# Performance work log

Hardware: AMD Instinct MI355X
Metric: run time of the kernel (lower is better)

## Reference

```python
import jax, jax.numpy as jnp
import numpy as np

EPS = 1e-5
HEADS = 4


def _ln(x, s, b):
    m = jnp.mean(x, axis=-1, keepdims=True)
    v = jnp.mean(jnp.square(x - m), axis=-1, keepdims=True)
    return (x - m) * jax.lax.rsqrt(v + EPS) * s + b


def _gru(x, Wg, bg, Wcx, bcx, Wch, bch):
    # In this GRUCell the gates depend only on the inputs, so the gate and
    # candidate_x matmuls are precomputed over all timesteps; only the
    # (reset*h) @ Wch matmul is sequential.
    gx = jax.nn.sigmoid(x @ Wg + bg)   # [B,S,2H]
    cx = x @ Wcx + bcx                 # [B,S,H]
    H = Wch.shape[0]

    def step(h, gc):
        g, c = gc
        r, u = jnp.split(g, 2, axis=-1)
        cand = jnp.tanh(c + (r * h) @ Wch + bch)
        h_new = u * h + (1.0 - u) * cand
        return h_new, h_new

    h0 = jnp.zeros((x.shape[0], H), x.dtype)
    _, ys = jax.lax.scan(step, h0, (gx.transpose(1, 0, 2), cx.transpose(1, 0, 2)))
    return ys.transpose(1, 0, 2)


def _attn(x, s, b, Wq, bq, Wk, bk, Wv, bv, Wo, bo):
    skip = x
    xn = _ln(x, s, b)
    B, S, _ = xn.shape
    QKV = Wq.shape[1]
    hd = QKV // HEADS
    q = (xn @ Wq + bq).reshape(B, S, HEADS, hd)
    k = (xn @ Wk + bk).reshape(B, S, HEADS, hd)
    v = (xn @ Wv + bv).reshape(B, S, HEADS, hd)
    scores = jnp.einsum('bqhd,bkhd->bhqk', q, k) / jnp.sqrt(jnp.asarray(hd, x.dtype))
    probs = jax.nn.softmax(scores, axis=-1)
    o = jnp.einsum('bhqk,bkhd->bqhd', probs, v).reshape(B, S, QKV)
    return o @ Wo + bo + skip


def _forward(x_cgm, x_other, W_in, b_in, ln0_s, ln0_b,
             g0_Wg, g0_bg, g0_Wcx, g0_bcx, g0_Wch, g0_bch, ln1_s, ln1_b,
             g1_Wg, g1_bg, g1_Wcx, g1_bcx, g1_Wch, g1_bch, ln2_s, ln2_b,
             aln_s, aln_b, Wq, bq, Wk, bk, Wv, bv, Wo, bo,
             Wd1, bd1, lnd1_s, lnd1_b, Wd2, bd2, lnd2_s, lnd2_b, Wout, bout):
    # input projection + LN
    x = _ln(x_cgm @ W_in + b_in, ln0_s, ln0_b)
    # GRU block 0 (residual: dims match, 256==256)
    y = _gru(x, g0_Wg, g0_bg, g0_Wcx, g0_bcx, g0_Wch, g0_bch)
    x = _ln(y, ln1_s, ln1_b) + x
    # GRU block 1
    y = _gru(x, g1_Wg, g1_bg, g1_Wcx, g1_bcx, g1_Wch, g1_bch)
    x = _ln(y, ln2_s, ln2_b) + x
    # attention block after every 2nd GRU block
    x = _attn(x, aln_s, aln_b, Wq, bq, Wk, bk, Wv, bv, Wo, bo)
    # pool over time, concat static features, dense head (no residuals: dims differ)
    pooled = jnp.mean(x, axis=1)
    c = jnp.concatenate([pooled, x_other], axis=-1)
    c = _ln(jax.nn.relu(c @ Wd1 + bd1), lnd1_s, lnd1_b)
    c = _ln(jax.nn.relu(c @ Wd2 + bd2), lnd2_s, lnd2_b)
    return (c @ Wout + bout).squeeze(-1)


def setup_inputs() -> dict:
    key = jax.random.key(0)
    ks = iter(jax.random.split(key, 64))

    def nrm(shape, scale=1.0):
        return jax.random.normal(next(ks), shape, jnp.float32) * scale

    B, S, Fc, Fo, D, QKV = 64, 288, 16, 32, 256, 64
    inp = {
        'x_cgm': nrm((B, S, Fc)),
        'x_other': nrm((B, Fo)),
        'W_in': nrm((Fc, D), Fc ** -0.5), 'b_in': jnp.zeros((D,), jnp.float32),
        'ln0_s': jnp.ones((D,), jnp.float32), 'ln0_b': jnp.zeros((D,), jnp.float32),
    }
    for p in ('g0', 'g1'):
        inp[p + '_Wg'] = nrm((D, 2 * D), D ** -0.5)
        inp[p + '_bg'] = jnp.zeros((2 * D,), jnp.float32)
        inp[p + '_Wcx'] = nrm((D, D), D ** -0.5)
        inp[p + '_bcx'] = jnp.zeros((D,), jnp.float32)
        inp[p + '_Wch'] = nrm((D, D), D ** -0.5)
        inp[p + '_bch'] = jnp.zeros((D,), jnp.float32)
    for n in ('ln1', 'ln2', 'aln'):
        inp[n + '_s'] = jnp.ones((D,), jnp.float32)
        inp[n + '_b'] = jnp.zeros((D,), jnp.float32)
    for n in ('Wq', 'Wk', 'Wv'):
        inp[n] = nrm((D, QKV), D ** -0.5)
    for n in ('bq', 'bk', 'bv'):
        inp[n] = jnp.zeros((QKV,), jnp.float32)
    inp['Wo'] = nrm((QKV, D), QKV ** -0.5)
    inp['bo'] = jnp.zeros((D,), jnp.float32)
    inp['Wd1'] = nrm((D + Fo, 128), (D + Fo) ** -0.5)
    inp['bd1'] = jnp.zeros((128,), jnp.float32)
    inp['lnd1_s'] = jnp.ones((128,), jnp.float32)
    inp['lnd1_b'] = jnp.zeros((128,), jnp.float32)
    inp['Wd2'] = nrm((128, 64), 128 ** -0.5)
    inp['bd2'] = jnp.zeros((64,), jnp.float32)
    inp['lnd2_s'] = jnp.ones((64,), jnp.float32)
    inp['lnd2_b'] = jnp.zeros((64,), jnp.float32)
    inp['Wout'] = nrm((64, 1), 64 ** -0.5)
    inp['bout'] = jnp.zeros((1,), jnp.float32)
    return inp


def reference(x_cgm, x_other, W_in, b_in, ln0_s, ln0_b,
              g0_Wg, g0_bg, g0_Wcx, g0_bcx, g0_Wch, g0_bch, ln1_s, ln1_b,
              g1_Wg, g1_bg, g1_Wcx, g1_bcx, g1_Wch, g1_bch, ln2_s, ln2_b,
              aln_s, aln_b, Wq, bq, Wk, bk, Wv, bv, Wo, bo,
              Wd1, bd1, lnd1_s, lnd1_b, Wd2, bd2, lnd2_s, lnd2_b, Wout, bout):
    return _forward(x_cgm, x_other, W_in, b_in, ln0_s, ln0_b,
                    g0_Wg, g0_bg, g0_Wcx, g0_bcx, g0_Wch, g0_bch, ln1_s, ln1_b,
                    g1_Wg, g1_bg, g1_Wcx, g1_bcx, g1_Wch, g1_bch, ln2_s, ln2_b,
                    aln_s, aln_b, Wq, bq, Wk, bk, Wv, bv, Wo, bo,
                    Wd1, bd1, lnd1_s, lnd1_b, Wd2, bd2, lnd2_s, lnd2_b, Wout, bout)
```

## Files before the change

### kernel.cpp

```cpp
#include <hip/hip_runtime.h>
#include <hip/hip_bf16.h>
#include <math.h>


#define EPS 1e-5f
constexpr int B_ = 64, S_ = 288, FC = 16, FO = 32, D_ = 256, QKVN = 64, HD = 16;
constexpr int TOK = B_ * S_;
constexpr int NX = TOK * D_;
constexpr int NG = TOK * 512;

typedef short bf16x8 __attribute__((ext_vector_type(8)));
typedef float f32x4 __attribute__((ext_vector_type(4)));

__device__ __forceinline__ short f2bf(float f) {
  __hip_bfloat16 h = __float2bfloat16(f);
  return __builtin_bit_cast(short, h);
}

__device__ __forceinline__ float blk_sum(float v, float* sc) {
  #pragma unroll
  for (int o = 32; o > 0; o >>= 1) v += __shfl_down(v, o, 64);
  int tid = threadIdx.x;
  int wid = tid >> 6, nw = blockDim.x >> 6;
  __syncthreads();
  if ((tid & 63) == 0) sc[wid] = v;
  __syncthreads();
  float s = 0.f;
  for (int w = 0; w < nw; ++w) s += sc[w];
  return s;
}

__global__ __launch_bounds__(256) void inproj_ln(
    const float* __restrict__ xc, const float* __restrict__ Wi,
    const float* __restrict__ bi, const float* __restrict__ sc_,
    const float* __restrict__ bb, float* __restrict__ X) {
  __shared__ float sc[8];
  int tok = blockIdx.x, j = threadIdx.x;
  const float* xr = xc + tok * FC;
  float acc = bi[j];
  #pragma unroll
  for (int i = 0; i < FC; ++i) acc += xr[i] * Wi[i * D_ + j];
  float m = blk_sum(acc, sc) * (1.f / D_);
  float d = acc - m;
  float var = blk_sum(d * d, sc) * (1.f / D_);
  X[tok * D_ + j] = d * rsqrtf(var + EPS) * sc_[j] + bb[j];
}

__global__ __launch_bounds__(256) void ln_token_res(
    const float* __restrict__ in, const float* __restrict__ sc_,
    const float* __restrict__ bb, const float* __restrict__ resid,
    float* __restrict__ out) {
  __shared__ float sc[8];
  int tok = blockIdx.x, j = threadIdx.x;
  float v = in[tok * D_ + j];
  float m = blk_sum(v, sc) * (1.f / D_);
  float d = v - m;
  float var = blk_sum(d * d, sc) * (1.f / D_);
  out[tok * D_ + j] = d * rsqrtf(var + EPS) * sc_[j] + bb[j] + resid[tok * D_ + j];
}

__global__ __launch_bounds__(256) void ln_ln(
    const float* __restrict__ Y, const float* __restrict__ s2,
    const float* __restrict__ b2, float* __restrict__ X,
    const float* __restrict__ sa, const float* __restrict__ ba,
    float* __restrict__ O) {
  __shared__ float sc[8];
  int tok = blockIdx.x, j = threadIdx.x;
  float v = Y[tok * D_ + j];
  float m = blk_sum(v, sc) * (1.f / D_);
  float d = v - m;
  float var = blk_sum(d * d, sc) * (1.f / D_);
  float r = d * rsqrtf(var + EPS) * s2[j] + b2[j] + X[tok * D_ + j];
  X[tok * D_ + j] = r;
  float m2 = blk_sum(r, sc) * (1.f / D_);
  float d2 = r - m2;
  float var2 = blk_sum(d2 * d2, sc) * (1.f / D_);
  O[tok * D_ + j] = d2 * rsqrtf(var2 + EPS) * sa[j] + ba[j];
}

template <int BN>
__device__ __forceinline__ void gemm_body(
    const float* __restrict__ A, const float* __restrict__ W,
    const float* __restrict__ bias, const float* __restrict__ resid,
    float* __restrict__ OUT, int N, int bn0, int K, int act, int res,
    short* As, short* Bs) {
  constexpr int BT = BN * 8 / 256;
  constexpr int NT16 = BN / 16;
  int tid = threadIdx.x;
  int wave = tid >> 6, lane = tid & 63;
  int quad = lane >> 4, m16 = lane & 15;
  int row0 = blockIdx.x * 128;
  const float* Ag = A + (size_t)row0 * K;

  f32x4 acc[2][NT16];
  #pragma unroll
  for (int mt = 0; mt < 2; ++mt)
    #pragma unroll
    for (int nt = 0; nt < NT16; ++nt) acc[mt][nt] = (f32x4){0.f, 0.f, 0.f, 0.f};

  float aR[4][8];
  float bR[BT][8];

  auto loadA = [&](int kk) {
    #pragma unroll
    for (int i = 0; i < 4; ++i) {
      int idx = tid + i * 256;
      int r = idx >> 3, oct = idx & 7;
      const float* p = Ag + (size_t)r * K + kk + oct * 8;
      float4 x = *(const float4*)p;
      float4 y = *(const float4*)(p + 4);
      aR[i][0] = x.x; aR[i][1] = x.y; aR[i][2] = x.z; aR[i][3] = x.w;
      aR[i][4] = y.x; aR[i][5] = y.y; aR[i][6] = y.z; aR[i][7] = y.w;
    }
  };
  auto loadB = [&](int kk) {
    #pragma unroll
    for (int i = 0; i < BT; ++i) {
      int idx = tid + i * 256;
      int n = idx & (BN - 1), oct = idx / BN;
      const float* p = W + (size_t)(kk + oct * 8) * N + bn0 + n;
      #pragma unroll
      for (int j = 0; j < 8; ++j) bR[i][j] = p[(size_t)j * N];
    }
  };
  auto storeA = [&]() {
    #pragma unroll
    for (int i = 0; i < 4; ++i) {
      int idx = tid + i * 256;
      int r = idx >> 3, oct = idx & 7;
      bf16x8 v;
      #pragma unroll
      for (int j = 0; j < 8; ++j) v[j] = f2bf(aR[i][j]);
      *(bf16x8*)&As[r * 72 + oct * 8] = v;
    }
  };
  auto storeB = [&]() {
    #pragma unroll
    for (int i = 0; i < BT; ++i) {
      int idx = tid + i * 256;
      int n = idx & (BN - 1), oct = idx / BN;
      bf16x8 v;
      #pragma unroll
      for (int j = 0; j < 8; ++j) v[j] = f2bf(bR[i][j]);
      *(bf16x8*)&Bs[n * 72 + oct * 8] = v;
    }
  };

  loadA(0); loadB(0);
  for (int kk = 0; kk < K; kk += 64) {
    storeA(); storeB();
    __builtin_amdgcn_s_waitcnt(0xC07F);
    __builtin_amdgcn_s_barrier();
    if (kk + 64 < K) { loadA(kk + 64); loadB(kk + 64); }
    #pragma unroll
    for (int kc = 0; kc < 2; ++kc) {
      bf16x8 af0 = *(const bf16x8*)&As[(wave * 32 + m16) * 72 + kc * 32 + quad * 8];
      bf16x8 af1 = *(const bf16x8*)&As[(wave * 32 + 16 + m16) * 72 + kc * 32 + quad * 8];
      #pragma unroll
      for (int nt = 0; nt < NT16; ++nt) {
        bf16x8 bfr = *(const bf16x8*)&Bs[(nt * 16 + m16) * 72 + kc * 32 + quad * 8];
        acc[0][nt] = __builtin_amdgcn_mfma_f32_16x16x32_bf16(af0, bfr, acc[0][nt], 0, 0, 0);
        acc[1][nt] = __builtin_amdgcn_mfma_f32_16x16x32_bf16(af1, bfr, acc[1][nt], 0, 0, 0);
      }
    }
    __builtin_amdgcn_s_waitcnt(0xC07F);
    __builtin_amdgcn_s_barrier();
  }
  #pragma unroll
  for (int mt = 0; mt < 2; ++mt) {
    #pragma unroll
    for (int nt = 0; nt < NT16; ++nt) {
      int col = bn0 + nt * 16 + m16;
      float bv = bias[col];
      #pragma unroll
      for (int r = 0; r < 4; ++r) {
        int row = row0 + wave * 32 + mt * 16 + quad * 4 + r;
        float v = acc[mt][nt][r] + bv;
        if (act) v = 1.f / (1.f + __expf(-v));
        if (res) v += resid[(size_t)row * N + col];
        OUT[(size_t)row * N + col] = v;
      }
    }
  }
}

__global__ __launch_bounds__(256) void gemm_gru(
    const float* __restrict__ A, const float* __restrict__ Wg,
    const float* __restrict__ bg, const float* __restrict__ Wc,
    const float* __restrict__ bc, float* __restrict__ G,
    float* __restrict__ Cc) {
  __shared__ short As[128 * 72];
  __shared__ short Bs[128 * 72];
  bool isG = blockIdx.y < 4;
  gemm_body<128>(A, isG ? Wg : Wc, isG ? bg : bc, nullptr, isG ? G : Cc,
                 isG ? 512 : 256, (isG ? blockIdx.y : blockIdx.y - 4) * 128,
                 256, isG ? 1 : 0, 0, As, Bs);
}

__global__ __launch_bounds__(256) void gemm_qkv(
    const float* __restrict__ A, const float* __restrict__ Wq,
    const float* __restrict__ bq, const float* __restrict__ Wk,
    const float* __restrict__ bk, const float* __restrict__ Wv,
    const float* __restrict__ bv, float* __restrict__ Q,
    float* __restrict__ Kb, float* __restrict__ V) {
  __shared__ short As[128 * 72];
  __shared__ short Bs[64 * 72];
  int y = blockIdx.y;
  const float* W = (y == 0) ? Wq : (y == 1) ? Wk : Wv;
  const float* bi = (y == 0) ? bq : (y == 1) ? bk : bv;
  float* O = (y == 0) ? Q : (y == 1) ? Kb : V;
  gemm_body<64>(A, W, bi, nullptr, O, 64, 0, 256, 0, 0, As, Bs);
}

__global__ __launch_bounds__(256) void gemm_proj(
    const float* __restrict__ A, const float* __restrict__ W,
    const float* __restrict__ bi, const float* __restrict__ resid,
    float* __restrict__ O) {
  __shared__ short As[128 * 72];
  __shared__ short Bs[128 * 72];
  gemm_body<128>(A, W, bi, resid, O, 256, blockIdx.y * 128, 64, 0, 1, As, Bs);
}

__global__ __launch_bounds__(512, 2) void gru_scan(
    const float* __restrict__ G, const float* __restrict__ C,
    const float* __restrict__ Wch, const float* __restrict__ bch,
    float* __restrict__ Y) {
  __shared__ short vstage[2][256];
  int tid = threadIdx.x;
  int b = blockIdx.x;
  int wave = tid >> 6, lane = tid & 63;
  int quad = lane >> 4, m16 = lane & 15;
  int col0 = 32 * wave + m16;
  int col1 = col0 + 16;

  bf16x8 wfrag[2][8];
  #pragma unroll
  for (int tt = 0; tt < 2; ++tt) {
    int n = (tt == 0) ? col0 : col1;
    #pragma unroll
    for (int c = 0; c < 8; ++c) {
      const float* wp = Wch + (size_t)(32 * c + quad * 8) * D_ + n;
      bf16x8 w;
      #pragma unroll
      for (int j = 0; j < 8; ++j) w[j] = f2bf(wp[(size_t)j * D_]);
      wfrag[tt][c] = w;
    }
  }

  const float* Gp = G + (size_t)b * S_ * 512;
  const float* Cp = C + (size_t)b * S_ * 256;
  float* Yp = Y + (size_t)b * S_ * 256;

  float bch0 = bch[col0], bch1 = bch[col1];
  float h0 = 0.f, h1 = 0.f;

  float cu0[4], cu1[4], cc0[4], cc1[4], cr0[4], cr1[4];
  #pragma unroll
  for (int i = 0; i < 4; ++i) {
    cu0[i] = Gp[(size_t)i * 512 + 256 + col0];
    cu1[i] = Gp[(size_t)i * 512 + 256 + col1];
    cc0[i] = Cp[(size_t)i * 256 + col0];
    cc1[i] = Cp[(size_t)i * 256 + col1];
    cr0[i] = Gp[(size_t)(i + 1) * 512 + col0];
    cr1[i] = Gp[(size_t)(i + 1) * 512 + col1];
  }

  if (tid < 256) vstage[0][tid] = 0;
  __syncthreads();

  constexpr int NGRP = S_ / 4;
  for (int g = 0; g < NGRP; ++g) {
    int gn = (g + 1 < NGRP) ? g + 1 : NGRP - 1;
    const float* Gn = Gp + (size_t)gn * 4 * 512;
    const float* Cn = Cp + (size_t)gn * 4 * 256;
    float nu0[4], nu1[4], nc0[4], nc1[4], nr0[4], nr1[4];
    #pragma unroll
    for (int i = 0; i < 4; ++i) {
      nu0[i] = Gn[(size_t)i * 512 + 256 + col0];
      nu1[i] = Gn[(size_t)i * 512 + 256 + col1];
      nc0[i] = Cn[(size_t)i * 256 + col0];
      nc1[i] = Cn[(size_t)i * 256 + col1];
      int ri = (gn * 4 + i + 1 < S_) ? i + 1 : i;
      nr0[i] = Gn[(size_t)ri * 512 + col0];
      nr1[i] = Gn[(size_t)ri * 512 + col1];
    }
    #pragma unroll
    for (int i = 0; i < 4; ++i) {
      int t = g * 4 + i;
      int buf = t & 1;
      f32x4 A0[4], A1[4];
      #pragma unroll
      for (int j = 0; j < 4; ++j) {
        A0[j] = (f32x4){0.f, 0.f, 0.f, 0.f};
        A1[j] = (f32x4){0.f, 0.f, 0.f, 0.f};
      }
      #pragma unroll
      for (int p = 0; p < 2; ++p) {
        #pragma unroll
        for (int j = 0; j < 4; ++j) {
          int c = p * 4 + j;
          bf16x8 af = *(const bf16x8*)&vstage[buf][(c * 4 + quad) * 8];
          A0[j] = __builtin_amdgcn_mfma_f32_16x16x32_bf16(af, wfrag[0][c], A0[j], 0, 0, 0);
          A1[j] = __builtin_amdgcn_mfma_f32_16x16x32_bf16(af, wfrag[1][c], A1[j], 0, 0, 0);
        }
      }
      float s0 = cc0[i] + bch0 + ((A0[0][0] + A0[1][0]) + (A0[2][0] + A0[3][0]));
      float s1 = cc1[i] + bch1 + ((A1[0][0] + A1[1][0]) + (A1[2][0] + A1[3][0]));
      float e0 = __expf(2.f * s0), e1 = __expf(2.f * s1);
      float cand0 = 1.f - 2.f / (e0 + 1.f);
      float cand1 = 1.f - 2.f / (e1 + 1.f);
      h0 = cu0[i] * h0 + (1.f - cu0[i]) * cand0;
      h1 = cu1[i] * h1 + (1.f - cu1[i]) * cand1;
      short v0 = f2bf(cr0[i] * h0), v1 = f2bf(cr1[i] * h1);
      if (quad == 0) {
        Yp[(size_t)t * 256 + col0] = h0;
        Yp[(size_t)t * 256 + col1] = h1;
        vstage[buf ^ 1][col0] = v0;
        vstage[buf ^ 1][col1] = v1;
      }
      __builtin_amdgcn_s_waitcnt(0xC07F);
      __builtin_amdgcn_s_barrier();
    }
    #pragma unroll
    for (int i = 0; i < 4; ++i) {
      cu0[i] = nu0[i]; cu1[i] = nu1[i];
      cc0[i] = nc0[i]; cc1[i] = nc1[i];
      cr0[i] = nr0[i]; cr1[i] = nr1[i];
    }
  }
}

__global__ __launch_bounds__(320) void attn(
    const float* __restrict__ Q, const float* __restrict__ Kv,
    const float* __restrict__ V, float* __restrict__ AO) {
  __shared__ float Kl[S_ * HD];
  __shared__ float Vl[S_ * HD];
  int b = blockIdx.x, hh = blockIdx.y;
  int tid = threadIdx.x;
  int hoff = hh * HD;
  for (int idx = tid; idx < S_ * HD; idx += 320) {
    int row = idx >> 4, d = idx & 15;
    Kl[idx] = Kv[((size_t)(b * S_ + row)) * QKVN + hoff + d];
    Vl[idx] = V[((size_t)(b * S_ + row)) * QKVN + hoff + d];
  }
  __syncthreads();
  if (tid >= S_) return;
  const float* qp = Q + ((size_t)(b * S_ + tid)) * QKVN + hoff;
  float4 q0 = *(const float4*)(qp + 0);
  float4 q1 = *(const float4*)(qp + 4);
  float4 q2 = *(const float4*)(qp + 8);
  float4 q3 = *(const float4*)(qp + 12);
  float m = -1e30f, l = 0.f;
  float4 o0 = {0, 0, 0, 0}, o1 = {0, 0, 0, 0}, o2 = {0, 0, 0, 0},
         o3 = {0, 0, 0, 0};
  for (int k = 0; k < S_; ++k) {
    const float4* kp = (const float4*)&Kl[k * HD];
    float4 k0 = kp[0], k1 = kp[1], k2 = kp[2], k3 = kp[3];
    float s = q0.x * k0.x + q0.y * k0.y + q0.z * k0.z + q0.w * k0.w +
              q1.x * k1.x + q1.y * k1.y + q1.z * k1.z + q1.w * k1.w +
              q2.x * k2.x + q2.y * k2.y + q2.z * k2.z + q2.w * k2.w +
              q3.x * k3.x + q3.y * k3.y + q3.z * k3.z + q3.w * k3.w;
    s *= 0.25f;
    float mn = fmaxf(m, s);
    float corr = __expf(m - mn);
    float p = __expf(s - mn);
    l = l * corr + p;
    const float4* vp = (const float4*)&Vl[k * HD];
    float4 v0 = vp[0], v1 = vp[1], v2 = vp[2], v3 = vp[3];
    o0.x = o0.x * corr + p * v0.x; o0.y = o0.y * corr + p * v0.y;
    o0.z = o0.z * corr + p * v0.z; o0.w = o0.w * corr + p * v0.w;
    o1.x = o1.x * corr + p * v1.x; o1.y = o1.y * corr + p * v1.y;
    o1.z = o1.z * corr + p * v1.z; o1.w = o1.w * corr + p * v1.w;
    o2.x = o2.x * corr + p * v2.x; o2.y = o2.y * corr + p * v2.y;
    o2.z = o2.z * corr + p * v2.z; o2.w = o2.w * corr + p * v2.w;
    o3.x = o3.x * corr + p * v3.x; o3.y = o3.y * corr + p * v3.y;
    o3.z = o3.z * corr + p * v3.z; o3.w = o3.w * corr + p * v3.w;
    m = mn;
  }
  float inv = 1.f / l;
  float* op = AO + ((size_t)(b * S_ + tid)) * QKVN + hoff;
  float4 r0 = {o0.x * inv, o0.y * inv, o0.z * inv, o0.w * inv};
  float4 r1 = {o1.x * inv, o1.y * inv, o1.z * inv, o1.w * inv};
  float4 r2 = {o2.x * inv, o2.y * inv, o2.z * inv, o2.w * inv};
  float4 r3 = {o3.x * inv, o3.y * inv, o3.z * inv, o3.w * inv};
  ((float4*)op)[0] = r0; ((float4*)op)[1] = r1;
  ((float4*)op)[2] = r2; ((float4*)op)[3] = r3;
}

__global__ __launch_bounds__(256) void head(
    const float* __restrict__ X, const float* __restrict__ xo,
    const float* __restrict__ Wd1, const float* __restrict__ bd1,
    const float* __restrict__ s1, const float* __restrict__ b1,
    const float* __restrict__ Wd2, const float* __restrict__ bd2,
    const float* __restrict__ s2, const float* __restrict__ b2,
    const float* __restrict__ Wout, const float* __restrict__ bout,
    float* __restrict__ out) {
  __shared__ float c[D_ + FO];
  __shared__ float h1[128];
  __shared__ float sc[8];
  int b = blockIdx.x, tid = threadIdx.x;
  {
    float acc = 0.f;
    const float* xp = X + (size_t)b * S_ * D_ + tid;
    #pragma unroll 4
    for (int t = 0; t < S_; ++t) acc += xp[(size_t)t * D_];
    c[tid] = acc * (1.f / S_);
  }
  if (tid < FO) c[D_ + tid] = xo[b * FO + tid];
  __syncthreads();
  float v = 0.f;
  if (tid < 128) {
    v = bd1[tid];
    for (int k = 0; k < D_ + FO; ++k) v += c[k] * Wd1[k * 128 + tid];
    v = fmaxf(v, 0.f);
  }
  float m = blk_sum(tid < 128 ? v : 0.f, sc) * (1.f / 128.f);
  float d = v - m;
  float var = blk_sum(tid < 128 ? d * d : 0.f, sc) * (1.f / 128.f);
  if (tid < 128) h1[tid] = d * rsqrtf(var + EPS) * s1[tid] + b1[tid];
  __syncthreads();
  float v2 = 0.f;
  if (tid < 64) {
    v2 = bd2[tid];
    for (int k = 0; k < 128; ++k) v2 += h1[k] * Wd2[k * 64 + tid];
    v2 = fmaxf(v2, 0.f);
  }
  float m2 = blk_sum(tid < 64 ? v2 : 0.f, sc) * (1.f / 64.f);
  float d2v = v2 - m2;
  float var2 = blk_sum(tid < 64 ? d2v * d2v : 0.f, sc) * (1.f / 64.f);
  float hv = (tid < 64) ? (d2v * rsqrtf(var2 + EPS) * s2[tid] + b2[tid]) : 0.f;
  float p = (tid < 64) ? hv * Wout[tid] : 0.f;
  float tot = blk_sum(p, sc);
  if (tid == 0) out[b] = tot + bout[0];
}

extern "C" void kernel_launch(void* const* d_in, const int* in_sizes, int n_in,
                              void* d_out, int out_size, void* d_ws,
                              size_t ws_size, hipStream_t stream) {
  const float* x_cgm = (const float*)d_in[0];
  const float* x_other = (const float*)d_in[1];
  const float* W_in = (const float*)d_in[2];
  const float* b_in = (const float*)d_in[3];
  const float* ln0_s = (const float*)d_in[4];
  const float* ln0_b = (const float*)d_in[5];
  const float* g0_Wg = (const float*)d_in[6];
  const float* g0_bg = (const float*)d_in[7];
  const float* g0_Wcx = (const float*)d_in[8];
  const float* g0_bcx = (const float*)d_in[9];
  const float* g0_Wch = (const float*)d_in[10];
  const float* g0_bch = (const float*)d_in[11];
  const float* g1_Wg = (const float*)d_in[12];
  const float* g1_bg = (const float*)d_in[13];
  const float* g1_Wcx = (const float*)d_in[14];
  const float* g1_bcx = (const float*)d_in[15];
  const float* g1_Wch = (const float*)d_in[16];
  const float* g1_bch = (const float*)d_in[17];
  const float* ln1_s = (const float*)d_in[18];
  const float* ln1_b = (const float*)d_in[19];
  const float* ln2_s = (const float*)d_in[20];
  const float* ln2_b = (const float*)d_in[21];
  const float* aln_s = (const float*)d_in[22];
  const float* aln_b = (const float*)d_in[23];
  const float* Wq = (const float*)d_in[24];
  const float* Wk = (const float*)d_in[25];
  const float* Wv = (const float*)d_in[26];
  const float* bq = (const float*)d_in[27];
  const float* bk = (const float*)d_in[28];
  const float* bv = (const float*)d_in[29];
  const float* Wo = (const float*)d_in[30];
  const float* bo = (const float*)d_in[31];
  const float* Wd1 = (const float*)d_in[32];
  const float* bd1 = (const float*)d_in[33];
  const float* lnd1_s = (const float*)d_in[34];
  const float* lnd1_b = (const float*)d_in[35];
  const float* Wd2 = (const float*)d_in[36];
  const float* bd2 = (const float*)d_in[37];
  const float* lnd2_s = (const float*)d_in[38];
  const float* lnd2_b = (const float*)d_in[39];
  const float* Wout = (const float*)d_in[40];
  const float* bout = (const float*)d_in[41];
  (void)in_sizes; (void)n_in; (void)out_size; (void)ws_size;

  float* ws = (float*)d_ws;
  float* X = ws;
  float* Yb = ws + NX;
  float* Gb = ws + 2 * NX;
  float* Cb = Gb + NG;
  float* Qb = Gb;
  float* Kb = Gb + TOK * QKVN;
  float* Vb = Gb + 2 * TOK * QKVN;
  float* AO = Cb;

  const int MB = TOK / 128;

  inproj_ln<<<TOK, 256, 0, stream>>>(x_cgm, W_in, b_in, ln0_s, ln0_b, X);

  gemm_gru<<<dim3(MB, 6), 256, 0, stream>>>(X, g0_Wg, g0_bg, g0_Wcx, g0_bcx, Gb, Cb);
  gru_scan<<<B_, 512, 0, stream>>>(Gb, Cb, g0_Wch, g0_bch, Yb);
  ln_token_res<<<TOK, 256, 0, stream>>>(Yb, ln1_s, ln1_b, X, X);

  gemm_gru<<<dim3(MB, 6), 256, 0, stream>>>(X, g1_Wg, g1_bg, g1_Wcx, g1_bcx, Gb, Cb);
  gru_scan<<<B_, 512, 0, stream>>>(Gb, Cb, g1_Wch, g1_bch, Yb);

  ln_ln<<<TOK, 256, 0, stream>>>(Yb, ln2_s, ln2_b, X, aln_s, aln_b, Yb);

  gemm_qkv<<<dim3(MB, 3), 256, 0, stream>>>(Yb, Wq, bq, Wk, bk, Wv, bv, Qb, Kb, Vb);
  attn<<<dim3(B_, 4), 320, 0, stream>>>(Qb, Kb, Vb, AO);
  gemm_proj<<<dim3(MB, 2), 256, 0, stream>>>(AO, Wo, bo, X, X);

  head<<<B_, 256, 0, stream>>>(X, x_other, Wd1, bd1, lnd1_s, lnd1_b,
                               Wd2, bd2, lnd2_s, lnd2_b, Wout, bout,
                               (float*)d_out);
}
```

Before: 702.3 us.

## Store GRU gate/candidate and attention intermediates in bf16

Gate, candidate and attention-input/output intermediates are now written and read as bf16 instead of fp32. This halves the global memory traffic for these buffers, which feed the GEMMs and the sequential GRU scan. GEMM A-operands that are already bf16 skip the conversion step. The cost is lower precision in the precomputed sigmoid gates and candidates that enter the recurrence, and the workspace buffers are reassigned to new aliases.

```diff
diff --git a/kernel.cpp b/kernel.cpp
--- a/kernel.cpp
+++ b/kernel.cpp
@@ -15,6 +15,9 @@
 __device__ __forceinline__ short f2bf(float f) {
   __hip_bfloat16 h = __float2bfloat16(f);
   return __builtin_bit_cast(short, h);
+}
+__device__ __forceinline__ float b2f(__hip_bfloat16 h) {
+  return __bfloat162float(h);
 }
 
 __device__ __forceinline__ float blk_sum(float v, float* sc) {
@@ -63,7 +66,7 @@
     const float* __restrict__ Y, const float* __restrict__ s2,
     const float* __restrict__ b2, float* __restrict__ X,
     const float* __restrict__ sa, const float* __restrict__ ba,
-    float* __restrict__ O) {
+    __hip_bfloat16* __restrict__ O) {
   __shared__ float sc[8];
   int tok = blockIdx.x, j = threadIdx.x;
   float v = Y[tok * D_ + j];
@@ -75,14 +78,14 @@
   float m2 = blk_sum(r, sc) * (1.f / D_);
   float d2 = r - m2;
   float var2 = blk_sum(d2 * d2, sc) * (1.f / D_);
-  O[tok * D_ + j] = d2 * rsqrtf(var2 + EPS) * sa[j] + ba[j];
-}
-
-template <int BN>
+  O[tok * D_ + j] = __float2bfloat16(d2 * rsqrtf(var2 + EPS) * sa[j] + ba[j]);
+}
+
+template <int BN, typename AT, int OBF>
 __device__ __forceinline__ void gemm_body(
-    const float* __restrict__ A, const float* __restrict__ W,
+    const AT* __restrict__ A, const float* __restrict__ W,
     const float* __restrict__ bias, const float* __restrict__ resid,
-    float* __restrict__ OUT, int N, int bn0, int K, int act, int res,
+    void* __restrict__ OUTv, int N, int bn0, int K, int act, int res,
     short* As, short* Bs) {
   constexpr int BT = BN * 8 / 256;
   constexpr int NT16 = BN / 16;
@@ -90,7 +93,7 @@
   int wave = tid >> 6, lane = tid & 63;
   int quad = lane >> 4, m16 = lane & 15;
   int row0 = blockIdx.x * 128;
-  const float* Ag = A + (size_t)row0 * K;
+  const AT* Ag = A + (size_t)row0 * K;
 
   f32x4 acc[2][NT16];
   #pragma unroll
@@ -98,7 +101,8 @@
     #pragma unroll
     for (int nt = 0; nt < NT16; ++nt) acc[mt][nt] = (f32x4){0.f, 0.f, 0.f, 0.f};
 
-  float aR[4][8];
+  float aRf[4][8];
+  bf16x8 aRb[4];
   float bR[BT][8];
 
   auto loadA = [&](int kk) {
@@ -106,11 +110,17 @@
     for (int i = 0; i < 4; ++i) {
       int idx = tid + i * 256;
       int r = idx >> 3, oct = idx & 7;
-      const float* p = Ag + (size_t)r * K + kk + oct * 8;
-      float4 x = *(const float4*)p;
-      float4 y = *(const float4*)(p + 4);
-      aR[i][0] = x.x; aR[i][1] = x.y; aR[i][2] = x.z; aR[i][3] = x.w;
-      aR[i][4] = y.x; aR[i][5] = y.y; aR[i][6] = y.z; aR[i][7] = y.w;
+      if constexpr (sizeof(AT) == 4) {
+        const float* p = (const float*)Ag + (size_t)r * K + kk + oct * 8;
+        float4 x = *(const float4*)p;
+        float4 y = *(const float4*)(p + 4);
+        aRf[i][0] = x.x; aRf[i][1] = x.y; aRf[i][2] = x.z; aRf[i][3] = x.w;
+        aRf[i][4] = y.x; aRf[i][5] = y.y; aRf[i][6] = y.z; aRf[i][7] = y.w;
+      } else {
+        const __hip_bfloat16* p =
+            (const __hip_bfloat16*)Ag + (size_t)r * K + kk + oct * 8;
+        aRb[i] = *(const bf16x8*)p;
+      }
     }
   };
   auto loadB = [&](int kk) {
@@ -128,10 +138,14 @@
     for (int i = 0; i < 4; ++i) {
       int idx = tid + i * 256;
       int r = idx >> 3, oct = idx & 7;
-      bf16x8 v;
-      #pragma unroll
-      for (int j = 0; j < 8; ++j) v[j] = f2bf(aR[i][j]);
-      *(bf16x8*)&As[r * 72 + oct * 8] = v;
+      if constexpr (sizeof(AT) == 4) {
+        bf16x8 v;
+        #pragma unroll
+        for (int j = 0; j < 8; ++j) v[j] = f2bf(aRf[i][j]);
+        *(bf16x8*)&As[r * 72 + oct * 8] = v;
+      } else {
+        *(bf16x8*)&As[r * 72 + oct * 8] = aRb[i];
+      }
     }
   };
   auto storeB = [&]() {
@@ -178,7 +192,11 @@
         float v = acc[mt][nt][r] + bv;
         if (act) v = 1.f / (1.f + __expf(-v));
         if (res) v += resid[(size_t)row * N + col];
-        OUT[(size_t)row * N + col] = v;
+        if constexpr (OBF) {
+          ((__hip_bfloat16*)OUTv)[(size_t)row * N + col] = __float2bfloat16(v);
+        } else {
+          ((float*)OUTv)[(size_t)row * N + col] = v;
+        }
       }
     }
   }
@@ -187,18 +205,19 @@
 __global__ __launch_bounds__(256) void gemm_gru(
     const float* __restrict__ A, const float* __restrict__ Wg,
     const float* __restrict__ bg, const float* __restrict__ Wc,
-    const float* __restrict__ bc, float* __restrict__ G,
-    float* __restrict__ Cc) {
+    const float* __restrict__ bc, __hip_bfloat16* __restrict__ G,
+    __hip_bfloat16* __restrict__ Cc) {
   __shared__ short As[128 * 72];
   __shared__ short Bs[128 * 72];
   bool isG = blockIdx.y < 4;
-  gemm_body<128>(A, isG ? Wg : Wc, isG ? bg : bc, nullptr, isG ? G : Cc,
-                 isG ? 512 : 256, (isG ? blockIdx.y : blockIdx.y - 4) * 128,
-                 256, isG ? 1 : 0, 0, As, Bs);
+  gemm_body<128, float, 1>(A, isG ? Wg : Wc, isG ? bg : bc, nullptr,
+                           isG ? (void*)G : (void*)Cc, isG ? 512 : 256,
+                           (isG ? blockIdx.y : blockIdx.y - 4) * 128, 256,
+                           isG ? 1 : 0, 0, As, Bs);
 }
 
 __global__ __launch_bounds__(256) void gemm_qkv(
-    const float* __restrict__ A, const float* __restrict__ Wq,
+    const __hip_bfloat16* __restrict__ A, const float* __restrict__ Wq,
     const float* __restrict__ bq, const float* __restrict__ Wk,
     const float* __restrict__ bk, const float* __restrict__ Wv,
     const float* __restrict__ bv, float* __restrict__ Q,
@@ -209,20 +228,21 @@
   const float* W = (y == 0) ? Wq : (y == 1) ? Wk : Wv;
   const float* bi = (y == 0) ? bq : (y == 1) ? bk : bv;
   float* O = (y == 0) ? Q : (y == 1) ? Kb : V;
-  gemm_body<64>(A, W, bi, nullptr, O, 64, 0, 256, 0, 0, As, Bs);
+  gemm_body<64, __hip_bfloat16, 0>(A, W, bi, nullptr, O, 64, 0, 256, 0, 0, As, Bs);
 }
 
 __global__ __launch_bounds__(256) void gemm_proj(
-    const float* __restrict__ A, const float* __restrict__ W,
+    const __hip_bfloat16* __restrict__ A, const float* __restrict__ W,
     const float* __restrict__ bi, const float* __restrict__ resid,
     float* __restrict__ O) {
   __shared__ short As[128 * 72];
   __shared__ short Bs[128 * 72];
-  gemm_body<128>(A, W, bi, resid, O, 256, blockIdx.y * 128, 64, 0, 1, As, Bs);
+  gemm_body<128, __hip_bfloat16, 0>(A, W, bi, resid, O, 256, blockIdx.y * 128,
+                                    64, 0, 1, As, Bs);
 }
 
 __global__ __launch_bounds__(512, 2) void gru_scan(
-    const float* __restrict__ G, const float* __restrict__ C,
+    const __hip_bfloat16* __restrict__ G, const __hip_bfloat16* __restrict__ C,
     const float* __restrict__ Wch, const float* __restrict__ bch,
     float* __restrict__ Y) {
   __shared__ short vstage[2][256];
@@ -247,8 +267,8 @@
     }
   }
 
-  const float* Gp = G + (size_t)b * S_ * 512;
-  const float* Cp = C + (size_t)b * S_ * 256;
+  const __hip_bfloat16* Gp = G + (size_t)b * S_ * 512;
+  const __hip_bfloat16* Cp = C + (size_t)b * S_ * 256;
   float* Yp = Y + (size_t)b * S_ * 256;
 
   float bch0 = bch[col0], bch1 = bch[col1];
@@ -257,12 +277,12 @@
   float cu0[4], cu1[4], cc0[4], cc1[4], cr0[4], cr1[4];
   #pragma unroll
   for (int i = 0; i < 4; ++i) {
-    cu0[i] = Gp[(size_t)i * 512 + 256 + col0];
-    cu1[i] = Gp[(size_t)i * 512 + 256 + col1];
-    cc0[i] = Cp[(size_t)i * 256 + col0];
-    cc1[i] = Cp[(size_t)i * 256 + col1];
-    cr0[i] = Gp[(size_t)(i + 1) * 512 + col0];
-    cr1[i] = Gp[(size_t)(i + 1) * 512 + col1];
+    cu0[i] = b2f(Gp[(size_t)i * 512 + 256 + col0]);
+    cu1[i] = b2f(Gp[(size_t)i * 512 + 256 + col1]);
+    cc0[i] = b2f(Cp[(size_t)i * 256 + col0]);
+    cc1[i] = b2f(Cp[(size_t)i * 256 + col1]);
+    cr0[i] = b2f(Gp[(size_t)(i + 1) * 512 + col0]);
+    cr1[i] = b2f(Gp[(size_t)(i + 1) * 512 + col1]);
   }
 
   if (tid < 256) vstage[0][tid] = 0;
@@ -271,18 +291,18 @@
   constexpr int NGRP = S_ / 4;
   for (int g = 0; g < NGRP; ++g) {
     int gn = (g + 1 < NGRP) ? g + 1 : NGRP - 1;
-    const float* Gn = Gp + (size_t)gn * 4 * 512;
-    const float* Cn = Cp + (size_t)gn * 4 * 256;
+    const __hip_bfloat16* Gn = Gp + (size_t)gn * 4 * 512;
+    const __hip_bfloat16* Cn = Cp + (size_t)gn * 4 * 256;
     float nu0[4], nu1[4], nc0[4], nc1[4], nr0[4], nr1[4];
     #pragma unroll
     for (int i = 0; i < 4; ++i) {
-      nu0[i] = Gn[(size_t)i * 512 + 256 + col0];
-      nu1[i] = Gn[(size_t)i * 512 + 256 + col1];
-      nc0[i] = Cn[(size_t)i * 256 + col0];
-      nc1[i] = Cn[(size_t)i * 256 + col1];
+      nu0[i] = b2f(Gn[(size_t)i * 512 + 256 + col0]);
+      nu1[i] = b2f(Gn[(size_t)i * 512 + 256 + col1]);
+      nc0[i] = b2f(Cn[(size_t)i * 256 + col0]);
+      nc1[i] = b2f(Cn[(size_t)i * 256 + col1]);
       int ri = (gn * 4 + i + 1 < S_) ? i + 1 : i;
-      nr0[i] = Gn[(size_t)ri * 512 + col0];
-      nr1[i] = Gn[(size_t)ri * 512 + col1];
+      nr0[i] = b2f(Gn[(size_t)ri * 512 + col0]);
+      nr1[i] = b2f(Gn[(size_t)ri * 512 + col1]);
     }
     #pragma unroll
     for (int i = 0; i < 4; ++i) {
@@ -332,7 +352,7 @@
 
 __global__ __launch_bounds__(320) void attn(
     const float* __restrict__ Q, const float* __restrict__ Kv,
-    const float* __restrict__ V, float* __restrict__ AO) {
+    const float* __restrict__ V, __hip_bfloat16* __restrict__ AO) {
   __shared__ float Kl[S_ * HD];
   __shared__ float Vl[S_ * HD];
   int b = blockIdx.x, hh = blockIdx.y;
@@ -378,13 +398,18 @@
     m = mn;
   }
   float inv = 1.f / l;
-  float* op = AO + ((size_t)(b * S_ + tid)) * QKVN + hoff;
-  float4 r0 = {o0.x * inv, o0.y * inv, o0.z * inv, o0.w * inv};
-  float4 r1 = {o1.x * inv, o1.y * inv, o1.z * inv, o1.w * inv};
-  float4 r2 = {o2.x * inv, o2.y * inv, o2.z * inv, o2.w * inv};
-  float4 r3 = {o3.x * inv, o3.y * inv, o3.z * inv, o3.w * inv};
-  ((float4*)op)[0] = r0; ((float4*)op)[1] = r1;
-  ((float4*)op)[2] = r2; ((float4*)op)[3] = r3;
+  __hip_bfloat16* op = AO + ((size_t)(b * S_ + tid)) * QKVN + hoff;
+  bf16x8 w0, w1;
+  w0[0] = f2bf(o0.x * inv); w0[1] = f2bf(o0.y * inv);
+  w0[2] = f2bf(o0.z * inv); w0[3] = f2bf(o0.w * inv);
+  w0[4] = f2bf(o1.x * inv); w0[5] = f2bf(o1.y * inv);
+  w0[6] = f2bf(o1.z * inv); w0[7] = f2bf(o1.w * inv);
+  w1[0] = f2bf(o2.x * inv); w1[1] = f2bf(o2.y * inv);
+  w1[2] = f2bf(o2.z * inv); w1[3] = f2bf(o2.w * inv);
+  w1[4] = f2bf(o3.x * inv); w1[5] = f2bf(o3.y * inv);
+  w1[6] = f2bf(o3.z * inv); w1[7] = f2bf(o3.w * inv);
+  *(bf16x8*)op = w0;
+  *(bf16x8*)(op + 8) = w1;
 }
 
 __global__ __launch_bounds__(256) void head(
@@ -484,12 +509,13 @@
   float* ws = (float*)d_ws;
   float* X = ws;
   float* Yb = ws + NX;
-  float* Gb = ws + 2 * NX;
-  float* Cb = Gb + NG;
-  float* Qb = Gb;
-  float* Kb = Gb + TOK * QKVN;
-  float* Vb = Gb + 2 * TOK * QKVN;
-  float* AO = Cb;
+  __hip_bfloat16* Gb = (__hip_bfloat16*)(ws + 2 * NX);
+  __hip_bfloat16* Cb = (__hip_bfloat16*)(ws + 2 * NX + NG);
+  float* Qb = ws + 2 * NX;
+  float* Kbuf = Qb + TOK * QKVN;
+  float* Vbuf = Qb + 2 * TOK * QKVN;
+  __hip_bfloat16* Obuf = Cb;
+  __hip_bfloat16* AO = (__hip_bfloat16*)Yb;
 
   const int MB = TOK / 128;
 
@@ -502,10 +528,11 @@
   gemm_gru<<<dim3(MB, 6), 256, 0, stream>>>(X, g1_Wg, g1_bg, g1_Wcx, g1_bcx, Gb, Cb);
   gru_scan<<<B_, 512, 0, stream>>>(Gb, Cb, g1_Wch, g1_bch, Yb);
 
-  ln_ln<<<TOK, 256, 0, stream>>>(Yb, ln2_s, ln2_b, X, aln_s, aln_b, Yb);
-
-  gemm_qkv<<<dim3(MB, 3), 256, 0, stream>>>(Yb, Wq, bq, Wk, bk, Wv, bv, Qb, Kb, Vb);
-  attn<<<dim3(B_, 4), 320, 0, stream>>>(Qb, Kb, Vb, AO);
+  ln_ln<<<TOK, 256, 0, stream>>>(Yb, ln2_s, ln2_b, X, aln_s, aln_b, Obuf);
+
+  gemm_qkv<<<dim3(MB, 3), 256, 0, stream>>>(Obuf, Wq, bq, Wk, bk, Wv, bv,
+                                            Qb, Kbuf, Vbuf);
+  attn<<<dim3(B_, 4), 320, 0, stream>>>(Qb, Kbuf, Vbuf, AO);
   gemm_proj<<<dim3(MB, 2), 256, 0, stream>>>(AO, Wo, bo, X, X);
 
   head<<<B_, 256, 0, stream>>>(X, x_other, Wd1, bd1, lnd1_s, lnd1_b,
```

Measured after the change: 710.4 us. About the same (+1.1%).
